# Optimization experiments

Measured on AMD Instinct MI355X. Metric: run time of the kernel, lower is better.

The kernel has to match this reference:

```python
import jax, jax.numpy as jnp
import numpy as np

R = 8  # number_of_remaining_feature_maps
NEG_SLOPE = 0.01  # torch LeakyReLU default


def setup_inputs() -> dict:
    key = jax.random.key(0)
    k0, k1, k2, k3, k4 = jax.random.split(key, 5)
    b, c, D, H, W = 8, 64, 48, 48, 48
    x = jax.random.normal(k0, (b, c, D, H, W), dtype=jnp.float32)
    s = 1.0 / np.sqrt(c)
    w1 = jax.random.uniform(k1, (c, c), jnp.float32, -s, s)
    b1 = jax.random.uniform(k2, (c,), jnp.float32, -s, s)
    w2 = jax.random.uniform(k3, (c, c), jnp.float32, -s, s)
    b2 = jax.random.uniform(k4, (c,), jnp.float32, -s, s)
    return {"x": x, "w1": w1, "b1": b1, "w2": w2, "b2": b2}


def reference(x, w1, b1, w2, b2):
    # x: (b, c, D, H, W)
    y = jnp.mean(x, axis=(2, 3, 4))                       # adaptive avg pool -> (b, c)
    y = jax.nn.leaky_relu(y @ w1.T + b1, NEG_SLOPE)       # Linear + LeakyReLU
    y = jax.nn.sigmoid(y @ w2.T + b2)                     # Linear + Sigmoid
    _, idx = jax.lax.top_k(y, R)                          # (b, R) channel indices
    # batched channel gather: (b, R, D, H, W)
    return jnp.take_along_axis(x, idx[:, :, None, None, None], axis=1)
```

## Files before the change

### kernel.cpp

```cpp
#include <hip/hip_runtime.h>
#include <math.h>

#define NCH 64
#define NB 8
#define RSEL 8
#define SPATIAL 110592
#define S4 27648
#define PARTS 4
#define CHUNK4 (S4 / PARTS)
#define ITERS (CHUNK4 / 256)
#define BATCH 9

typedef float f4 __attribute__((ext_vector_type(4)));

__global__ __launch_bounds__(256) void mean_kernel(const float* __restrict__ x,
                                                   float* __restrict__ partials) {
    const int bc   = blockIdx.x >> 2;
    const int part = blockIdx.x & 3;
    const f4* p = (const f4*)(x + (size_t)bc * SPATIAL) + part * CHUNK4 + threadIdx.x;
    float s = 0.f;
    #pragma unroll
    for (int r = 0; r < ITERS / BATCH; ++r) {
        f4 v[BATCH];
        #pragma unroll
        for (int i = 0; i < BATCH; ++i) v[i] = p[(r * BATCH + i) * 256];
        #pragma unroll
        for (int i = 0; i < BATCH; ++i) s += (v[i].x + v[i].y) + (v[i].z + v[i].w);
    }
    #pragma unroll
    for (int o = 32; o >= 1; o >>= 1) s += __shfl_down(s, o, 64);
    __shared__ float ws[4];
    const int lane = threadIdx.x & 63;
    const int wv   = threadIdx.x >> 6;
    if (lane == 0) ws[wv] = s;
    __syncthreads();
    if (threadIdx.x == 0) {
        partials[blockIdx.x] = (ws[0] + ws[1]) + (ws[2] + ws[3]);
    }
}

__global__ __launch_bounds__(64) void mlp_topk_kernel(const float* __restrict__ partials,
                                                      const float* __restrict__ w1,
                                                      const float* __restrict__ b1,
                                                      const float* __restrict__ w2,
                                                      const float* __restrict__ b2,
                                                      int* __restrict__ idx_out) {
    const int j = threadIdx.x;
    __shared__ float m[NB][NCH];
    __shared__ float h[NB][NCH];
    __shared__ float y[NB][NCH];

    #pragma unroll
    for (int b = 0; b < NB; ++b) {
        const float* pp = partials + (size_t)(b * NCH + j) * PARTS;
        m[b][j] = ((pp[0] + pp[1]) + (pp[2] + pp[3])) * (1.0f / (float)SPATIAL);
    }
    __syncthreads();

    float wrow[NCH];
    #pragma unroll 8
    for (int k = 0; k < NCH; ++k) wrow[k] = w1[j * NCH + k];
    float bj = b1[j];
    #pragma unroll
    for (int b = 0; b < NB; ++b) {
        float acc = bj;
        #pragma unroll 8
        for (int k = 0; k < NCH; ++k) acc += m[b][k] * wrow[k];
        h[b][j] = acc > 0.f ? acc : 0.01f * acc;
    }
    __syncthreads();

    #pragma unroll 8
    for (int k = 0; k < NCH; ++k) wrow[k] = w2[j * NCH + k];
    bj = b2[j];
    #pragma unroll
    for (int b = 0; b < NB; ++b) {
        float acc = bj;
        #pragma unroll 8
        for (int k = 0; k < NCH; ++k) acc += h[b][k] * wrow[k];
        y[b][j] = 1.0f / (1.0f + expf(-acc));
    }
    __syncthreads();

    for (int b = 0; b < NB; ++b) {
        float mine = y[b][j];
        #pragma unroll
        for (int r = 0; r < RSEL; ++r) {
            float v = mine;
            int   c = j;
            #pragma unroll
            for (int o = 32; o >= 1; o >>= 1) {
                float ov = __shfl_xor(v, o, 64);
                int   oc = __shfl_xor(c, o, 64);
                if (ov > v || (ov == v && oc < c)) { v = ov; c = oc; }
            }
            if (j == 0) idx_out[b * RSEL + r] = c;
            if (j == c) mine = -INFINITY;
        }
    }
}

__global__ __launch_bounds__(256) void gather_kernel(const float* __restrict__ x,
                                                     const int* __restrict__ idx,
                                                     float* __restrict__ out) {
    const int pair = blockIdx.y;
    const int b    = pair >> 3;
    const int ch   = idx[pair];
    const f4* src = (const f4*)(x + (size_t)(b * NCH + ch) * SPATIAL);
    f4*       dst = (f4*)(out + (size_t)pair * SPATIAL);
    const int base = blockIdx.x * 1024 + threadIdx.x;
    #pragma unroll
    for (int i = 0; i < 4; ++i) {
        f4 v = src[base + i * 256];
        __builtin_nontemporal_store(v, &dst[base + i * 256]);
    }
}

extern "C" void kernel_launch(void* const* d_in, const int* in_sizes, int n_in,
                              void* d_out, int out_size, void* d_ws, size_t ws_size,
                              hipStream_t stream) {
    const float* x  = (const float*)d_in[0];
    const float* w1 = (const float*)d_in[1];
    const float* b1 = (const float*)d_in[2];
    const float* w2 = (const float*)d_in[3];
    const float* b2 = (const float*)d_in[4];
    float* out = (float*)d_out;

    float* partials = (float*)d_ws;
    int*   idx      = (int*)((char*)d_ws + NB * NCH * PARTS * sizeof(float));

    mean_kernel<<<dim3(NB * NCH * PARTS), dim3(256), 0, stream>>>(x, partials);
    mlp_topk_kernel<<<dim3(1), dim3(64), 0, stream>>>(partials, w1, b1, w2, b2, idx);
    gather_kernel<<<dim3(S4 / 1024, NB * RSEL), dim3(256), 0, stream>>>(x, idx, out);
}
```

Baseline: 376.6 us.

## Widen MLP/top-k kernel to 256 threads with rank-based top-k selection

The single-block MLP+top-k kernel now runs with 256 threads instead of 64, and each wavefront computes two batch rows of both linear layers. Weight rows are loaded as float4 vectors. The serial shuffle-based argmax top-k is replaced by a parallel rank count, where each element counts how many larger values exist and writes itself if its rank is below R. This cuts the latency of a serial one-block stage sitting between two bandwidth-bound kernels. The kernel is tiny relative to the memory-bound mean and gather passes, so any overall effect is small.

```diff
diff --git a/kernel.cpp b/kernel.cpp
--- a/kernel.cpp
+++ b/kernel.cpp
@@ -39,64 +39,85 @@
     }
 }
 
-__global__ __launch_bounds__(64) void mlp_topk_kernel(const float* __restrict__ partials,
+__global__ __launch_bounds__(256) void mlp_topk_kernel(const float* __restrict__ partials,
                                                       const float* __restrict__ w1,
                                                       const float* __restrict__ b1,
                                                       const float* __restrict__ w2,
                                                       const float* __restrict__ b2,
                                                       int* __restrict__ idx_out) {
-    const int j = threadIdx.x;
+    const int t  = threadIdx.x;
+    const int j  = t & 63;
+    const int wv = t >> 6;
+    const int ba = 2 * wv;
+    const int bb = ba + 1;
+
     __shared__ float m[NB][NCH];
     __shared__ float h[NB][NCH];
     __shared__ float y[NB][NCH];
 
+    const f4* wr1 = (const f4*)(w1 + (size_t)j * NCH);
+    f4 wvreg[16];
     #pragma unroll
-    for (int b = 0; b < NB; ++b) {
-        const float* pp = partials + (size_t)(b * NCH + j) * PARTS;
-        m[b][j] = ((pp[0] + pp[1]) + (pp[2] + pp[3])) * (1.0f / (float)SPATIAL);
+    for (int q = 0; q < 16; ++q) wvreg[q] = wr1[q];
+    const float bias1 = b1[j];
+
+    #pragma unroll
+    for (int i = 0; i < 2; ++i) {
+        const int e = t + i * 256;
+        const float* pp = partials + (size_t)e * PARTS;
+        m[e >> 6][e & 63] = ((pp[0] + pp[1]) + (pp[2] + pp[3])) * (1.0f / (float)SPATIAL);
     }
     __syncthreads();
 
-    float wrow[NCH];
-    #pragma unroll 8
-    for (int k = 0; k < NCH; ++k) wrow[k] = w1[j * NCH + k];
-    float bj = b1[j];
-    #pragma unroll
-    for (int b = 0; b < NB; ++b) {
-        float acc = bj;
-        #pragma unroll 8
-        for (int k = 0; k < NCH; ++k) acc += m[b][k] * wrow[k];
-        h[b][j] = acc > 0.f ? acc : 0.01f * acc;
+    {
+        float a0 = bias1, a1 = bias1;
+        #pragma unroll
+        for (int q = 0; q < 16; ++q) {
+            #pragma unroll
+            for (int s = 0; s < 4; ++s) {
+                const float wk = ((const float*)&wvreg[q])[s];
+                a0 += m[ba][q * 4 + s] * wk;
+                a1 += m[bb][q * 4 + s] * wk;
+            }
+        }
+        h[ba][j] = a0 > 0.f ? a0 : 0.01f * a0;
+        h[bb][j] = a1 > 0.f ? a1 : 0.01f * a1;
     }
     __syncthreads();
 
-    #pragma unroll 8
-    for (int k = 0; k < NCH; ++k) wrow[k] = w2[j * NCH + k];
-    bj = b2[j];
-    #pragma unroll
-    for (int b = 0; b < NB; ++b) {
-        float acc = bj;
-        #pragma unroll 8
-        for (int k = 0; k < NCH; ++k) acc += h[b][k] * wrow[k];
-        y[b][j] = 1.0f / (1.0f + expf(-acc));
+    {
+        const f4* wr2 = (const f4*)(w2 + (size_t)j * NCH);
+        #pragma unroll
+        for (int q = 0; q < 16; ++q) wvreg[q] = wr2[q];
+        const float bias2 = b2[j];
+        float a0 = bias2, a1 = bias2;
+        #pragma unroll
+        for (int q = 0; q < 16; ++q) {
+            #pragma unroll
+            for (int s = 0; s < 4; ++s) {
+                const float wk = ((const float*)&wvreg[q])[s];
+                a0 += h[ba][q * 4 + s] * wk;
+                a1 += h[bb][q * 4 + s] * wk;
+            }
+        }
+        y[ba][j] = 1.0f / (1.0f + expf(-a0));
+        y[bb][j] = 1.0f / (1.0f + expf(-a1));
     }
     __syncthreads();
 
-    for (int b = 0; b < NB; ++b) {
-        float mine = y[b][j];
+    #pragma unroll
+    for (int i = 0; i < 2; ++i) {
+        const int e  = t + i * 256;
+        const int eb = e >> 6;
+        const int ej = e & 63;
+        const float mine = y[eb][ej];
+        int rank = 0;
         #pragma unroll
-        for (int r = 0; r < RSEL; ++r) {
-            float v = mine;
-            int   c = j;
-            #pragma unroll
-            for (int o = 32; o >= 1; o >>= 1) {
-                float ov = __shfl_xor(v, o, 64);
-                int   oc = __shfl_xor(c, o, 64);
-                if (ov > v || (ov == v && oc < c)) { v = ov; c = oc; }
-            }
-            if (j == 0) idx_out[b * RSEL + r] = c;
-            if (j == c) mine = -INFINITY;
+        for (int k = 0; k < NCH; ++k) {
+            const float v = y[eb][k];
+            rank += (int)((v > mine) | ((v == mine) & (k < ej)));
         }
+        if (rank < RSEL) idx_out[eb * RSEL + rank] = ej;
     }
 }
 
@@ -130,6 +151,6 @@
     int*   idx      = (int*)((char*)d_ws + NB * NCH * PARTS * sizeof(float));
 
     mean_kernel<<<dim3(NB * NCH * PARTS), dim3(256), 0, stream>>>(x, partials);
-    mlp_topk_kernel<<<dim3(1), dim3(64), 0, stream>>>(partials, w1, b1, w2, b2, idx);
+    mlp_topk_kernel<<<dim3(1), dim3(256), 0, stream>>>(partials, w1, b1, w2, b2, idx);
     gather_kernel<<<dim3(S4 / 1024, NB * RSEL), dim3(256), 0, stream>>>(x, idx, out);
 }
```

Result: faster. 331.3 us (-12.0%).

## Fuse MLP and top-k into gather kernel, recomputing per block

Applied to the files above, without the earlier changes.

Removes the single-block MLP/top-k kernel and folds its work into every gather block. Each block recomputes the two 64x64 linear layers for its batch element, then finds its channel by rank counting rather than a repeated wave-shuffle argmax. This drops one launch and the serial single-wave stage between the mean and the gather. In exchange, the MLP is computed redundantly across 27x64 blocks, and each block waits on that compute before issuing its copy loads.

```diff
diff --git a/kernel.cpp b/kernel.cpp
--- a/kernel.cpp
+++ b/kernel.cpp
@@ -39,76 +39,76 @@
     }
 }
 
-__global__ __launch_bounds__(64) void mlp_topk_kernel(const float* __restrict__ partials,
-                                                      const float* __restrict__ w1,
-                                                      const float* __restrict__ b1,
-                                                      const float* __restrict__ w2,
-                                                      const float* __restrict__ b2,
-                                                      int* __restrict__ idx_out) {
-    const int j = threadIdx.x;
-    __shared__ float m[NB][NCH];
-    __shared__ float h[NB][NCH];
-    __shared__ float y[NB][NCH];
+__global__ __launch_bounds__(256) void mlp_gather_kernel(const float* __restrict__ x,
+                                                         const float* __restrict__ partials,
+                                                         const float* __restrict__ w1,
+                                                         const float* __restrict__ b1,
+                                                         const float* __restrict__ w2,
+                                                         const float* __restrict__ b2,
+                                                         float* __restrict__ out) {
+    const int pair = blockIdx.y;
+    const int b    = pair >> 3;
+    const int r    = pair & 7;
+    const int t    = threadIdx.x;
 
-    #pragma unroll
-    for (int b = 0; b < NB; ++b) {
-        const float* pp = partials + (size_t)(b * NCH + j) * PARTS;
-        m[b][j] = ((pp[0] + pp[1]) + (pp[2] + pp[3])) * (1.0f / (float)SPATIAL);
+    __shared__ float m_s[NCH];
+    __shared__ float h_s[NCH];
+    __shared__ float y_s[NCH];
+    __shared__ int   ch_s;
+
+    f4 wreg[16];
+    float bias = 0.f;
+    if (t < NCH) {
+        const f4* wr = (const f4*)(w1 + (size_t)t * NCH);
+        #pragma unroll
+        for (int q = 0; q < 16; ++q) wreg[q] = wr[q];
+        bias = b1[t];
+        const f4 pv = ((const f4*)partials)[b * NCH + t];
+        m_s[t] = ((pv.x + pv.y) + (pv.z + pv.w)) * (1.0f / (float)SPATIAL);
     }
     __syncthreads();
 
-    float wrow[NCH];
-    #pragma unroll 8
-    for (int k = 0; k < NCH; ++k) wrow[k] = w1[j * NCH + k];
-    float bj = b1[j];
-    #pragma unroll
-    for (int b = 0; b < NB; ++b) {
-        float acc = bj;
-        #pragma unroll 8
-        for (int k = 0; k < NCH; ++k) acc += m[b][k] * wrow[k];
-        h[b][j] = acc > 0.f ? acc : 0.01f * acc;
+    if (t < NCH) {
+        float acc = bias;
+        #pragma unroll
+        for (int q = 0; q < 16; ++q) {
+            acc += m_s[4 * q + 0] * wreg[q].x + m_s[4 * q + 1] * wreg[q].y +
+                   m_s[4 * q + 2] * wreg[q].z + m_s[4 * q + 3] * wreg[q].w;
+        }
+        h_s[t] = acc > 0.f ? acc : 0.01f * acc;
     }
     __syncthreads();
 
-    #pragma unroll 8
-    for (int k = 0; k < NCH; ++k) wrow[k] = w2[j * NCH + k];
-    bj = b2[j];
-    #pragma unroll
-    for (int b = 0; b < NB; ++b) {
-        float acc = bj;
-        #pragma unroll 8
-        for (int k = 0; k < NCH; ++k) acc += h[b][k] * wrow[k];
-        y[b][j] = 1.0f / (1.0f + expf(-acc));
+    if (t < NCH) {
+        const f4* wr = (const f4*)(w2 + (size_t)t * NCH);
+        #pragma unroll
+        for (int q = 0; q < 16; ++q) wreg[q] = wr[q];
+        float acc = b2[t];
+        #pragma unroll
+        for (int q = 0; q < 16; ++q) {
+            acc += h_s[4 * q + 0] * wreg[q].x + h_s[4 * q + 1] * wreg[q].y +
+                   h_s[4 * q + 2] * wreg[q].z + h_s[4 * q + 3] * wreg[q].w;
+        }
+        y_s[t] = 1.0f / (1.0f + expf(-acc));
     }
     __syncthreads();
 
-    for (int b = 0; b < NB; ++b) {
-        float mine = y[b][j];
+    if (t < NCH) {
+        const float mine = y_s[t];
+        int rank = 0;
         #pragma unroll
-        for (int r = 0; r < RSEL; ++r) {
-            float v = mine;
-            int   c = j;
-            #pragma unroll
-            for (int o = 32; o >= 1; o >>= 1) {
-                float ov = __shfl_xor(v, o, 64);
-                int   oc = __shfl_xor(c, o, 64);
-                if (ov > v || (ov == v && oc < c)) { v = ov; c = oc; }
-            }
-            if (j == 0) idx_out[b * RSEL + r] = c;
-            if (j == c) mine = -INFINITY;
+        for (int k = 0; k < NCH; ++k) {
+            const float v = y_s[k];
+            rank += (int)((v > mine) | ((v == mine) & (k < t)));
         }
+        if (rank == r) ch_s = t;
     }
-}
+    __syncthreads();
 
-__global__ __launch_bounds__(256) void gather_kernel(const float* __restrict__ x,
-                                                     const int* __restrict__ idx,
-                                                     float* __restrict__ out) {
-    const int pair = blockIdx.y;
-    const int b    = pair >> 3;
-    const int ch   = idx[pair];
+    const int ch = ch_s;
     const f4* src = (const f4*)(x + (size_t)(b * NCH + ch) * SPATIAL);
     f4*       dst = (f4*)(out + (size_t)pair * SPATIAL);
-    const int base = blockIdx.x * 1024 + threadIdx.x;
+    const int base = blockIdx.x * 1024 + t;
     #pragma unroll
     for (int i = 0; i < 4; ++i) {
         f4 v = src[base + i * 256];
@@ -127,9 +127,8 @@
     float* out = (float*)d_out;
 
     float* partials = (float*)d_ws;
-    int*   idx      = (int*)((char*)d_ws + NB * NCH * PARTS * sizeof(float));
 
     mean_kernel<<<dim3(NB * NCH * PARTS), dim3(256), 0, stream>>>(x, partials);
-    mlp_topk_kernel<<<dim3(1), dim3(64), 0, stream>>>(partials, w1, b1, w2, b2, idx);
-    gather_kernel<<<dim3(S4 / 1024, NB * RSEL), dim3(256), 0, stream>>>(x, idx, out);
+    mlp_gather_kernel<<<dim3(S4 / 1024, NB * RSEL), dim3(256), 0, stream>>>(
+        x, partials, w1, b1, w2, b2, out);
 }
```

New measurement: 329.7 us. 12.4% less time.
